# Kernel tuning notes

Measured on AMD Instinct MI355X. Metric: run time of the kernel, lower is better.

Reference implementation:

```python
import jax, jax.numpy as jnp
import numpy as np

IN_FEATURES, OUT_FEATURES, KERNEL_DIMS = 1024, 128, 8
BATCH = 256


def setup_inputs() -> dict:
    key = jax.random.key(0)
    kx, kT = jax.random.split(key)
    x = jax.random.normal(kx, (BATCH, IN_FEATURES), dtype=jnp.float32)
    T = jax.random.normal(kT, (IN_FEATURES, OUT_FEATURES, KERNEL_DIMS), dtype=jnp.float32)
    return {"x": x, "T": T}


def reference(x, T):
    B = x.shape[0]
    in_f, out_f, kd = T.shape
    # M: (B, out_features, kernel_dims)
    M = (x @ T.reshape(in_f, out_f * kd)).reshape(B, out_f, kd)
    # pairwise L1 distance over kernel dims: (B, B, out_features)
    diffs = jnp.abs(M[None, :, :, :] - M[:, None, :, :]).sum(axis=3)
    # similarity features: sum over other samples, subtract self-term (exp(0)=1)
    c = jnp.exp(-diffs).sum(axis=1) - 1.0  # (B, out_features)
    return jnp.concatenate([x, c], axis=1)
```

## Files before the change

kernel.cpp:

```cpp
#include <hip/hip_runtime.h>
#include <hip/hip_bf16.h>
#include <stdint.h>

#define BATCH 256
#define INF   1024
#define OUTF  128
#define KD    8
#define NN    1024
#define OROW  1152

typedef __attribute__((ext_vector_type(8))) short short8;
typedef __attribute__((ext_vector_type(4))) float f32x4;

__device__ __forceinline__ unsigned short f2bf(float f) {
    union { float f; uint32_t u; } v; v.f = f;
    uint32_t r = v.u + 0x7FFFu + ((v.u >> 16) & 1u);
    return (unsigned short)(r >> 16);
}

__global__ __launch_bounds__(256) void prep_kernel(
    const float* __restrict__ x, const float* __restrict__ T,
    float* __restrict__ out, unsigned short* __restrict__ xbf,
    unsigned short* __restrict__ Tt)
{
    __shared__ unsigned short lds[64 * 65];
    int bid = blockIdx.x;
    int t = threadIdx.x;
    if (bid < 256) {
        int i0 = (bid >> 4) << 6;
        int n0 = (bid & 15) << 6;
        int tx = t & 63, ty = t >> 6;
        for (int r = ty; r < 64; r += 4) {
            float v = T[(size_t)(i0 + r) * NN + n0 + tx];
            lds[tx * 65 + r] = f2bf(v);
        }
        __syncthreads();
        for (int p = 0; p < 8; ++p) {
            int q = p * 512 + t * 2;
            int n = q >> 6, i = q & 63;
            uint32_t u = (uint32_t)lds[n * 65 + i] | ((uint32_t)lds[n * 65 + i + 1] << 16);
            *(uint32_t*)(Tt + (size_t)(n0 + n) * INF + i0 + i) = u;
        }
    } else {
        int bx = bid - 256;
        for (int p = 0; p < 4; ++p) {
            int a = bx * 4 + p;
            int j = t * 4;
            float4 v = *(const float4*)(x + (size_t)a * INF + j);
            *(float4*)(out + (size_t)a * OROW + j) = v;
            uint2 u;
            u.x = (uint32_t)f2bf(v.x) | ((uint32_t)f2bf(v.y) << 16);
            u.y = (uint32_t)f2bf(v.z) | ((uint32_t)f2bf(v.w) << 16);
            *(uint2*)(xbf + (size_t)a * INF + j) = u;
        }
        for (int s = t; s < 512; s += 256) {
            int f = bx * 512 + s;
            int a = f >> 7, o = f & 127;
            out[(size_t)a * OROW + INF + o] = -1.0f;
        }
    }
}

__global__ __launch_bounds__(128) void gemm_kernel(
    const unsigned short* __restrict__ xbf,
    const unsigned short* __restrict__ Tt,
    float* __restrict__ M)
{
    __shared__ float lds[64 * 16];
    int bid = blockIdx.x;
    int a0 = (bid & 7) << 5;
    int n0 = (bid >> 3) << 5;
    int t = threadIdx.x;
    int wave = t >> 6, lane = t & 63;
    int rc = lane & 15, quad = lane >> 4;
    int k0 = wave * 512 + quad * 8;

    f32x4 acc[2][2] = {{{0.f,0.f,0.f,0.f},{0.f,0.f,0.f,0.f}},
                       {{0.f,0.f,0.f,0.f},{0.f,0.f,0.f,0.f}}};
    const unsigned short* pa0 = xbf + (size_t)(a0 + rc) * INF + k0;
    const unsigned short* pa1 = pa0 + 16 * INF;
    const unsigned short* pb0 = Tt + (size_t)(n0 + rc) * INF + k0;
    const unsigned short* pb1 = pb0 + 16 * INF;
#pragma unroll 4
    for (int s = 0; s < 16; ++s) {
        int k = s * 32;
        short8 af0 = *(const short8*)(pa0 + k);
        short8 af1 = *(const short8*)(pa1 + k);
        short8 bg0 = *(const short8*)(pb0 + k);
        short8 bg1 = *(const short8*)(pb1 + k);
        acc[0][0] = __builtin_amdgcn_mfma_f32_16x16x32_bf16(af0, bg0, acc[0][0], 0, 0, 0);
        acc[0][1] = __builtin_amdgcn_mfma_f32_16x16x32_bf16(af0, bg1, acc[0][1], 0, 0, 0);
        acc[1][0] = __builtin_amdgcn_mfma_f32_16x16x32_bf16(af1, bg0, acc[1][0], 0, 0, 0);
        acc[1][1] = __builtin_amdgcn_mfma_f32_16x16x32_bf16(af1, bg1, acc[1][1], 0, 0, 0);
    }
    if (wave == 1) {
        for (int h = 0; h < 2; ++h)
            for (int g = 0; g < 2; ++g)
                for (int r = 0; r < 4; ++r)
                    lds[lane * 16 + (h * 2 + g) * 4 + r] = acc[h][g][r];
    }
    __syncthreads();
    if (wave == 0) {
        for (int h = 0; h < 2; ++h)
            for (int g = 0; g < 2; ++g)
                for (int r = 0; r < 4; ++r) {
                    float v = acc[h][g][r] + lds[lane * 16 + (h * 2 + g) * 4 + r];
                    int rr = a0 + h * 16 + quad * 4 + r;
                    int cc = n0 + g * 16 + rc;
                    M[(size_t)rr * NN + cc] = v;
                }
    }
}

__global__ __launch_bounds__(256) void pair_kernel(
    const float* __restrict__ M, float* __restrict__ out)
{
    int o = blockIdx.x >> 1;
    int half = blockIdx.x & 1;
    int a = threadIdx.x;
    const float* ma = M + (size_t)a * NN + o * KD;
    float4 m0 = *(const float4*)(ma);
    float4 m1 = *(const float4*)(ma + 4);
    float ssum = 0.f;
    int b0 = half * 128;
#pragma unroll 4
    for (int b = b0; b < b0 + 128; ++b) {
        const float* mb = M + (size_t)b * NN + o * KD;
        float4 q0 = *(const float4*)(mb);
        float4 q1 = *(const float4*)(mb + 4);
        float d = fabsf(m0.x - q0.x) + fabsf(m0.y - q0.y)
                + fabsf(m0.z - q0.z) + fabsf(m0.w - q0.w)
                + fabsf(m1.x - q1.x) + fabsf(m1.y - q1.y)
                + fabsf(m1.z - q1.z) + fabsf(m1.w - q1.w);
        ssum += __expf(-d);
    }
    atomicAdd(out + (size_t)a * OROW + INF + o, ssum);
}

extern "C" void kernel_launch(void* const* d_in, const int* in_sizes, int n_in,
                              void* d_out, int out_size, void* d_ws, size_t ws_size,
                              hipStream_t stream) {
    const float* x = (const float*)d_in[0];
    const float* T = (const float*)d_in[1];
    float* out = (float*)d_out;
    unsigned short* xbf = (unsigned short*)d_ws;
    unsigned short* Tt  = (unsigned short*)((char*)d_ws + 524288);
    float*          M   = (float*)((char*)d_ws + 524288 + 2097152);

    prep_kernel<<<320, 256, 0, stream>>>(x, T, out, xbf, Tt);
    gemm_kernel<<<256, 128, 0, stream>>>(xbf, Tt, M);
    pair_kernel<<<256, 256, 0, stream>>>(M, out);
}
```

Baseline: 82.04 us.

## Fuse GEMM and pairwise-distance into one kernel per output feature

Replaces the separate T-transpose, GEMM and pair kernels with one kernel per (output feature, batch half). Each block converts its T slice to bf16 in LDS, computes the 256x8 M slice with MFMA, and runs the pairwise L1/exp sum out of LDS. This removes the global M round trip, the Tt buffer, the atomics and the -1 initialisation. The cost is that the GEMM for each feature is computed twice, once per batch half, and every block reads all of xbf.

```diff
diff --git a/kernel.cpp b/kernel.cpp
--- a/kernel.cpp
+++ b/kernel.cpp
@@ -8,6 +8,8 @@
 #define KD    8
 #define NN    1024
 #define OROW  1152
+#define BLP   1032
+#define MOP   10
 
 typedef __attribute__((ext_vector_type(8))) short short8;
 typedef __attribute__((ext_vector_type(4))) float f32x4;
@@ -17,124 +19,104 @@
     uint32_t r = v.u + 0x7FFFu + ((v.u >> 16) & 1u);
     return (unsigned short)(r >> 16);
 }
+__device__ __forceinline__ uint32_t pack2(float lo, float hi) {
+    return (uint32_t)f2bf(lo) | ((uint32_t)f2bf(hi) << 16);
+}
 
 __global__ __launch_bounds__(256) void prep_kernel(
-    const float* __restrict__ x, const float* __restrict__ T,
-    float* __restrict__ out, unsigned short* __restrict__ xbf,
-    unsigned short* __restrict__ Tt)
+    const float* __restrict__ x, float* __restrict__ out,
+    unsigned short* __restrict__ xbf)
 {
-    __shared__ unsigned short lds[64 * 65];
+    int g = (blockIdx.x * 256 + threadIdx.x) * 8;
+    int a = g >> 10, j = g & 1023;
+    float4 v0 = *(const float4*)(x + g);
+    float4 v1 = *(const float4*)(x + g + 4);
+    *(float4*)(out + (size_t)a * OROW + j)     = v0;
+    *(float4*)(out + (size_t)a * OROW + j + 4) = v1;
+    uint4 u;
+    u.x = pack2(v0.x, v0.y);
+    u.y = pack2(v0.z, v0.w);
+    u.z = pack2(v1.x, v1.y);
+    u.w = pack2(v1.z, v1.w);
+    *(uint4*)(xbf + g) = u;
+}
+
+__global__ __launch_bounds__(512) void fused_kernel(
+    const unsigned short* __restrict__ xbf,
+    const float* __restrict__ T,
+    float* __restrict__ out)
+{
+    __shared__ __align__(16) unsigned short Bl[8 * BLP];
+    __shared__ __align__(16) float Mo[256 * MOP];
+    __shared__ float lds_c[128 * 4];
     int bid = blockIdx.x;
+    int o = bid >> 1, ah = bid & 1;
     int t = threadIdx.x;
-    if (bid < 256) {
-        int i0 = (bid >> 4) << 6;
-        int n0 = (bid & 15) << 6;
-        int tx = t & 63, ty = t >> 6;
-        for (int r = ty; r < 64; r += 4) {
-            float v = T[(size_t)(i0 + r) * NN + n0 + tx];
-            lds[tx * 65 + r] = f2bf(v);
+
+    const float* Tb = T + o * 8;
+#pragma unroll
+    for (int p = 0; p < 4; ++p) {
+        int f = p * 512 + t;
+        int i = f >> 1;
+        int h = (f & 1) * 4;
+        float4 v = *(const float4*)(Tb + (size_t)i * NN + h);
+        Bl[(h + 0) * BLP + i] = f2bf(v.x);
+        Bl[(h + 1) * BLP + i] = f2bf(v.y);
+        Bl[(h + 2) * BLP + i] = f2bf(v.z);
+        Bl[(h + 3) * BLP + i] = f2bf(v.w);
+    }
+    __syncthreads();
+
+    int w = t >> 6, lane = t & 63, rc = lane & 15, quad = lane >> 4;
+    {
+        const unsigned short* pa0 = xbf + (size_t)(w * 32 + rc) * INF + quad * 8;
+        const unsigned short* pa1 = pa0 + 16 * INF;
+        const unsigned short* bl = Bl + (rc & 7) * BLP + quad * 8;
+        f32x4 acc0 = {0.f, 0.f, 0.f, 0.f}, acc1 = {0.f, 0.f, 0.f, 0.f};
+#pragma unroll 4
+        for (int s = 0; s < 32; ++s) {
+            short8 bf = *(const short8*)(bl + s * 32);
+            short8 a0 = *(const short8*)(pa0 + s * 32);
+            short8 a1 = *(const short8*)(pa1 + s * 32);
+            acc0 = __builtin_amdgcn_mfma_f32_16x16x32_bf16(a0, bf, acc0, 0, 0, 0);
+            acc1 = __builtin_amdgcn_mfma_f32_16x16x32_bf16(a1, bf, acc1, 0, 0, 0);
         }
-        __syncthreads();
-        for (int p = 0; p < 8; ++p) {
-            int q = p * 512 + t * 2;
-            int n = q >> 6, i = q & 63;
-            uint32_t u = (uint32_t)lds[n * 65 + i] | ((uint32_t)lds[n * 65 + i + 1] << 16);
-            *(uint32_t*)(Tt + (size_t)(n0 + n) * INF + i0 + i) = u;
-        }
-    } else {
-        int bx = bid - 256;
-        for (int p = 0; p < 4; ++p) {
-            int a = bx * 4 + p;
-            int j = t * 4;
-            float4 v = *(const float4*)(x + (size_t)a * INF + j);
-            *(float4*)(out + (size_t)a * OROW + j) = v;
-            uint2 u;
-            u.x = (uint32_t)f2bf(v.x) | ((uint32_t)f2bf(v.y) << 16);
-            u.y = (uint32_t)f2bf(v.z) | ((uint32_t)f2bf(v.w) << 16);
-            *(uint2*)(xbf + (size_t)a * INF + j) = u;
-        }
-        for (int s = t; s < 512; s += 256) {
-            int f = bx * 512 + s;
-            int a = f >> 7, o = f & 127;
-            out[(size_t)a * OROW + INF + o] = -1.0f;
+        if (rc < 8) {
+#pragma unroll
+            for (int r = 0; r < 4; ++r) {
+                Mo[(w * 32 + quad * 4 + r) * MOP + rc]      = acc0[r];
+                Mo[(w * 32 + 16 + quad * 4 + r) * MOP + rc] = acc1[r];
+            }
         }
     }
-}
+    __syncthreads();
 
-__global__ __launch_bounds__(128) void gemm_kernel(
-    const unsigned short* __restrict__ xbf,
-    const unsigned short* __restrict__ Tt,
-    float* __restrict__ M)
-{
-    __shared__ float lds[64 * 16];
-    int bid = blockIdx.x;
-    int a0 = (bid & 7) << 5;
-    int n0 = (bid >> 3) << 5;
-    int t = threadIdx.x;
-    int wave = t >> 6, lane = t & 63;
-    int rc = lane & 15, quad = lane >> 4;
-    int k0 = wave * 512 + quad * 8;
-
-    f32x4 acc[2][2] = {{{0.f,0.f,0.f,0.f},{0.f,0.f,0.f,0.f}},
-                       {{0.f,0.f,0.f,0.f},{0.f,0.f,0.f,0.f}}};
-    const unsigned short* pa0 = xbf + (size_t)(a0 + rc) * INF + k0;
-    const unsigned short* pa1 = pa0 + 16 * INF;
-    const unsigned short* pb0 = Tt + (size_t)(n0 + rc) * INF + k0;
-    const unsigned short* pb1 = pb0 + 16 * INF;
+    int a_l = t & 127, q = t >> 7;
+    int a_g = ah * 128 + a_l;
+    float2 m0 = *(const float2*)&Mo[a_g * MOP + 0];
+    float2 m1 = *(const float2*)&Mo[a_g * MOP + 2];
+    float2 m2 = *(const float2*)&Mo[a_g * MOP + 4];
+    float2 m3 = *(const float2*)&Mo[a_g * MOP + 6];
+    float ssum = 0.f;
 #pragma unroll 4
-    for (int s = 0; s < 16; ++s) {
-        int k = s * 32;
-        short8 af0 = *(const short8*)(pa0 + k);
-        short8 af1 = *(const short8*)(pa1 + k);
-        short8 bg0 = *(const short8*)(pb0 + k);
-        short8 bg1 = *(const short8*)(pb1 + k);
-        acc[0][0] = __builtin_amdgcn_mfma_f32_16x16x32_bf16(af0, bg0, acc[0][0], 0, 0, 0);
-        acc[0][1] = __builtin_amdgcn_mfma_f32_16x16x32_bf16(af0, bg1, acc[0][1], 0, 0, 0);
-        acc[1][0] = __builtin_amdgcn_mfma_f32_16x16x32_bf16(af1, bg0, acc[1][0], 0, 0, 0);
-        acc[1][1] = __builtin_amdgcn_mfma_f32_16x16x32_bf16(af1, bg1, acc[1][1], 0, 0, 0);
-    }
-    if (wave == 1) {
-        for (int h = 0; h < 2; ++h)
-            for (int g = 0; g < 2; ++g)
-                for (int r = 0; r < 4; ++r)
-                    lds[lane * 16 + (h * 2 + g) * 4 + r] = acc[h][g][r];
-    }
-    __syncthreads();
-    if (wave == 0) {
-        for (int h = 0; h < 2; ++h)
-            for (int g = 0; g < 2; ++g)
-                for (int r = 0; r < 4; ++r) {
-                    float v = acc[h][g][r] + lds[lane * 16 + (h * 2 + g) * 4 + r];
-                    int rr = a0 + h * 16 + quad * 4 + r;
-                    int cc = n0 + g * 16 + rc;
-                    M[(size_t)rr * NN + cc] = v;
-                }
-    }
-}
-
-__global__ __launch_bounds__(256) void pair_kernel(
-    const float* __restrict__ M, float* __restrict__ out)
-{
-    int o = blockIdx.x >> 1;
-    int half = blockIdx.x & 1;
-    int a = threadIdx.x;
-    const float* ma = M + (size_t)a * NN + o * KD;
-    float4 m0 = *(const float4*)(ma);
-    float4 m1 = *(const float4*)(ma + 4);
-    float ssum = 0.f;
-    int b0 = half * 128;
-#pragma unroll 4
-    for (int b = b0; b < b0 + 128; ++b) {
-        const float* mb = M + (size_t)b * NN + o * KD;
-        float4 q0 = *(const float4*)(mb);
-        float4 q1 = *(const float4*)(mb + 4);
+    for (int it = 0; it < 64; ++it) {
+        int b = q * 64 + it;
+        float2 q0 = *(const float2*)&Mo[b * MOP + 0];
+        float2 q1 = *(const float2*)&Mo[b * MOP + 2];
+        float2 q2 = *(const float2*)&Mo[b * MOP + 4];
+        float2 q3 = *(const float2*)&Mo[b * MOP + 6];
         float d = fabsf(m0.x - q0.x) + fabsf(m0.y - q0.y)
-                + fabsf(m0.z - q0.z) + fabsf(m0.w - q0.w)
                 + fabsf(m1.x - q1.x) + fabsf(m1.y - q1.y)
-                + fabsf(m1.z - q1.z) + fabsf(m1.w - q1.w);
+                + fabsf(m2.x - q2.x) + fabsf(m2.y - q2.y)
+                + fabsf(m3.x - q3.x) + fabsf(m3.y - q3.y);
         ssum += __expf(-d);
     }
-    atomicAdd(out + (size_t)a * OROW + INF + o, ssum);
+    lds_c[a_l * 4 + q] = ssum;
+    __syncthreads();
+    if (t < 128) {
+        float4 v = *(const float4*)&lds_c[t * 4];
+        out[(size_t)(ah * 128 + t) * OROW + INF + o] = v.x + v.y + v.z + v.w - 1.0f;
+    }
 }
 
 extern "C" void kernel_launch(void* const* d_in, const int* in_sizes, int n_in,
@@ -144,10 +126,7 @@
     const float* T = (const float*)d_in[1];
     float* out = (float*)d_out;
     unsigned short* xbf = (unsigned short*)d_ws;
-    unsigned short* Tt  = (unsigned short*)((char*)d_ws + 524288);
-    float*          M   = (float*)((char*)d_ws + 524288 + 2097152);
 
-    prep_kernel<<<320, 256, 0, stream>>>(x, T, out, xbf, Tt);
-    gemm_kernel<<<256, 128, 0, stream>>>(xbf, Tt, M);
-    pair_kernel<<<256, 256, 0, stream>>>(M, out);
+    prep_kernel<<<128, 256, 0, stream>>>(x, out, xbf);
+    fused_kernel<<<256, 512, 0, stream>>>(xbf, T, out);
 }
```

New measurement: 84.80 us. 3.4% more time.
